# Kernel optimization log

Measured on AMD Instinct MI355X. Metric: run time of the kernel, lower is better.

Reference implementation:

```python
import jax, jax.numpy as jnp
import numpy as np

N, IN_DIM, OUT_DIM, HEADS, SUB = 4096, 256, 128, 4, 32
ETA = 0.5
LAMBDA_SPARSE = 0.05
NEG_BIG = -1e9


def setup_inputs() -> dict:
    key = jax.random.key(0)
    k1, k2, k3, k4 = jax.random.split(key, 4)
    H = jax.random.normal(k1, (N, IN_DIM), dtype=jnp.float32)
    # sparse binary adjacency mask (avg degree ~ 41) with self-loops
    adj_mask = (jax.random.uniform(k2, (N, N)) < 0.01).astype(jnp.float32)
    adj_mask = adj_mask.at[jnp.arange(N), jnp.arange(N)].set(1.0)
    # per-head orthonormal subspace bases U_k = QR(randn)[:, :SUB]
    raw = jax.random.normal(k3, (HEADS, IN_DIM, SUB), dtype=jnp.float32)
    U = jax.vmap(lambda r: jnp.linalg.qr(r)[0])(raw)  # [h, D, s]
    threshold = jnp.full((OUT_DIM,), LAMBDA_SPARSE, dtype=jnp.float32)
    proj_w = jax.random.normal(k4, (OUT_DIM, IN_DIM), dtype=jnp.float32) / np.float32(np.sqrt(IN_DIM))
    return {"H": H, "adj_mask": adj_mask, "U": U, "threshold": threshold, "proj_w": proj_w}


def reference(H, adj_mask, U, threshold, proj_w):
    # Z_k = U_k^T @ H^T  -> [h, s, N]
    Z = jnp.einsum('hds,nd->hsn', U, H)
    # scores_k = Z_k^T @ Z_k / sqrt(s)  -> [h, N, N]
    scores = jnp.einsum('hsn,hsm->hnm', Z, Z) / jnp.sqrt(jnp.float32(SUB))
    scores = scores + (1.0 - adj_mask)[None, :, :] * NEG_BIG
    alpha = jax.nn.softmax(scores, axis=-1)  # torch softmax(dim=1) on [N,N] rows
    # agg_k = Z_k @ alpha_k^T  -> [h, s, N];  sum_k U_k @ agg_k -> [D, N]
    agg = jnp.einsum('hsj,hij->hsi', Z, alpha)
    agg_sum = jnp.einsum('hds,hsn->dn', U, agg)
    H_half = H + ETA * agg_sum.T           # [N, D]
    H_half = H_half @ proj_w.T             # [N, out_dim]
    # soft-threshold
    H_out = jnp.sign(H_half) * jax.nn.relu(jnp.abs(H_half) - threshold[None, :])
    # orthogonality loss: sum_k ||U_k^T U_k - I||_F^2 + sum_{k<l} ||U_k^T U_l||_F^2
    G = jnp.einsum('kds,ldt->klst', U, U)  # [h, h, s, s]
    eye_s = jnp.eye(SUB, dtype=U.dtype)
    eye_h = jnp.eye(HEADS, dtype=U.dtype)
    sub = G - eye_h[:, :, None, None] * eye_s[None, None, :, :]
    sq = jnp.sum(sub ** 2, axis=(2, 3))    # [h, h]
    orth_loss = jnp.sum(jnp.triu(jnp.ones((HEADS, HEADS), dtype=U.dtype)) * sq)
    return H_out, orth_loss
```

## Files before the change

kernel.cpp:

```cpp
#include <hip/hip_runtime.h>
#include <hip/hip_bf16.h>
#include <math.h>

#define NN 4096
#define IN_DIM 256
#define OUT_DIM 128
#define HEADS 4
#define SUB 32
#define MAXDEG 128
#define ETA 0.5f
#define INV_SQRT_SUB 0.17677669529663687f

typedef __attribute__((ext_vector_type(8))) short bf16x8;
typedef __attribute__((ext_vector_type(4))) short s16x4;
typedef __attribute__((ext_vector_type(4))) float f32x4;

static __device__ inline short f2bf(float f) {
    unsigned u = __float_as_uint(f);
    unsigned r = u + 0x7FFFu + ((u >> 16) & 1u);
    return (short)(r >> 16);
}
static __device__ inline float bf2f(short s) {
    return __uint_as_float(((unsigned)(unsigned short)s) << 16);
}
#define MFMA16(a, b, c) __builtin_amdgcn_mfma_f32_16x16x32_bf16(a, b, c, 0, 0, 0)

__global__ __launch_bounds__(256) void fused_small(const float* __restrict__ U,
                                                   const float* __restrict__ PW,
                                                   const float* __restrict__ adj,
                                                   short* __restrict__ Wh,
                                                   short* __restrict__ Wl,
                                                   float* __restrict__ W2,
                                                   float* __restrict__ loss_parts,
                                                   int* __restrict__ nbr,
                                                   int* __restrict__ deg) {
    int b = blockIdx.x;
    int t = threadIdx.x;
    __shared__ float sh[260];
    __shared__ int cnt2[2];

    if (b < 256) {
        float v;
        if (b < 128) {
            int h = b >> 5, s = b & 31;
            v = U[h * IN_DIM * SUB + t * SUB + s];
        } else {
            v = PW[(b - 128) * IN_DIM + t];
        }
        short hi = f2bf(v);
        Wh[b * IN_DIM + t] = hi;
        Wl[b * IN_DIM + t] = f2bf(v - bf2f(hi));
    } else if (b < 384) {
        int hs = b - 256;
        int h = hs >> 5, s = hs & 31;
        sh[t] = U[h * IN_DIM * SUB + t * SUB + s];
        __syncthreads();
        if (t < 128) {
            const float4* pw4 = (const float4*)(PW + t * IN_DIM);
            const float4* u4  = (const float4*)sh;
            float acc = 0.f;
            #pragma unroll 4
            for (int d4 = 0; d4 < 64; ++d4) {
                float4 a = u4[d4], p = pw4[d4];
                acc += a.x * p.x + a.y * p.y + a.z * p.z + a.w * p.w;
            }
            W2[hs * OUT_DIM + t] = acc;
        }
    } else if (b < 394) {
        const int pk[10] = {0,0,0,0,1,1,1,2,2,3};
        const int pl[10] = {0,1,2,3,1,2,3,2,3,3};
        int p = b - 384;
        int k = pk[p], l = pl[p];
        int t2 = t & 31;
        int sg = t >> 5;
        const float* Uk = U + k * IN_DIM * SUB;
        const float* Ul = U + l * IN_DIM * SUB;
        float a0 = 0.f, a1 = 0.f, a2 = 0.f, a3 = 0.f;
        #pragma unroll 4
        for (int d = 0; d < IN_DIM; ++d) {
            float ul = Ul[d * SUB + t2];
            float u0 = Uk[d * SUB + sg * 4 + 0];
            float u1 = Uk[d * SUB + sg * 4 + 1];
            float u2 = Uk[d * SUB + sg * 4 + 2];
            float u3 = Uk[d * SUB + sg * 4 + 3];
            a0 += u0 * ul; a1 += u1 * ul; a2 += u2 * ul; a3 += u3 * ul;
        }
        if (k == l) {
            if (sg * 4 + 0 == t2) a0 -= 1.f;
            if (sg * 4 + 1 == t2) a1 -= 1.f;
            if (sg * 4 + 2 == t2) a2 -= 1.f;
            if (sg * 4 + 3 == t2) a3 -= 1.f;
        }
        float local = a0 * a0 + a1 * a1 + a2 * a2 + a3 * a3;
        local += __shfl_xor(local, 32, 64);
        local += __shfl_xor(local, 16, 64);
        local += __shfl_xor(local, 8, 64);
        local += __shfl_xor(local, 4, 64);
        local += __shfl_xor(local, 2, 64);
        local += __shfl_xor(local, 1, 64);
        if ((t & 63) == 0) sh[256 + (t >> 6)] = local;
        __syncthreads();
        if (t == 0) loss_parts[p] = sh[256] + sh[257] + sh[258] + sh[259];
    } else {
        int sb = b - 394;
        int half = t >> 7, u = t & 127;
        int row = sb * 2 + half;
        const float4* row4 = (const float4*)(adj + (size_t)row * NN);
        float4 v[8];
        #pragma unroll
        for (int k = 0; k < 8; ++k) v[k] = row4[u + k * 128];
        if (u == 0) cnt2[half] = 0;
        __syncthreads();
        int* nrow = nbr + row * MAXDEG;
        #pragma unroll
        for (int k = 0; k < 8; ++k) {
            int j0 = (u + k * 128) * 4;
            if (v[k].x > 0.5f) { int p = atomicAdd(&cnt2[half], 1); if (p < MAXDEG) nrow[p] = j0; }
            if (v[k].y > 0.5f) { int p = atomicAdd(&cnt2[half], 1); if (p < MAXDEG) nrow[p] = j0 + 1; }
            if (v[k].z > 0.5f) { int p = atomicAdd(&cnt2[half], 1); if (p < MAXDEG) nrow[p] = j0 + 2; }
            if (v[k].w > 0.5f) { int p = atomicAdd(&cnt2[half], 1); if (p < MAXDEG) nrow[p] = j0 + 3; }
        }
        __syncthreads();
        int dgr = cnt2[half] < MAXDEG ? cnt2[half] : MAXDEG;
        if (u >= dgr) nrow[u] = 0;
        if (u == 0) deg[row] = dgr;
    }
}

#define LDA 264
__global__ __launch_bounds__(256) void ztp_mfma(const float* __restrict__ H,
                                                const short* __restrict__ Wh,
                                                const short* __restrict__ Wl,
                                                float* __restrict__ ZT,
                                                float* __restrict__ P) {
    __shared__ short Ah[16 * LDA];
    __shared__ short Al[16 * LDA];
    int t = threadIdx.x, b = blockIdx.x;
    int m0 = (b >> 1) * 16, chalf = b & 1;

    {
        int r = t >> 4, dbase = (t & 15) * 16;
        const float4* src = (const float4*)(H + (size_t)(m0 + r) * IN_DIM + dbase);
        #pragma unroll
        for (int q = 0; q < 4; ++q) {
            float4 f = src[q];
            float fv[4] = {f.x, f.y, f.z, f.w};
            s16x4 hi, lo;
            #pragma unroll
            for (int j = 0; j < 4; ++j) {
                short h = f2bf(fv[j]);
                hi[j] = h;
                lo[j] = f2bf(fv[j] - bf2f(h));
            }
            *(s16x4*)&Ah[r * LDA + dbase + q * 4] = hi;
            *(s16x4*)&Al[r * LDA + dbase + q * 4] = lo;
        }
    }
    __syncthreads();

    int wave = t >> 6, lane = t & 63;
    int c0 = chalf * 128 + wave * 32;
    int arow = lane & 15, agrp = lane >> 4;

    const short* ahp = &Ah[arow * LDA + agrp * 8];
    const short* alp = &Al[arow * LDA + agrp * 8];
    const short* bh0 = Wh + (size_t)(c0 + arow) * IN_DIM + agrp * 8;
    const short* bl0 = Wl + (size_t)(c0 + arow) * IN_DIM + agrp * 8;
    const short* bh1 = bh0 + 16 * IN_DIM;
    const short* bl1 = bl0 + 16 * IN_DIM;

    f32x4 acc0 = {0.f, 0.f, 0.f, 0.f};
    f32x4 acc1 = {0.f, 0.f, 0.f, 0.f};

    #pragma unroll
    for (int kk = 0; kk < 8; ++kk) {
        int d0 = kk * 32;
        bf16x8 a_h = *(const bf16x8*)(ahp + d0);
        bf16x8 a_l = *(const bf16x8*)(alp + d0);
        bf16x8 b0h = *(const bf16x8*)(bh0 + d0);
        bf16x8 b0l = *(const bf16x8*)(bl0 + d0);
        bf16x8 b1h = *(const bf16x8*)(bh1 + d0);
        bf16x8 b1l = *(const bf16x8*)(bl1 + d0);
        acc0 = MFMA16(a_h, b0h, acc0);
        acc0 = MFMA16(a_h, b0l, acc0);
        acc0 = MFMA16(a_l, b0h, acc0);
        acc1 = MFMA16(a_h, b1h, acc1);
        acc1 = MFMA16(a_h, b1l, acc1);
        acc1 = MFMA16(a_l, b1h, acc1);
    }

    float* dst = chalf ? P : ZT;
    int colbase = c0 - chalf * 128;
    #pragma unroll
    for (int i = 0; i < 4; ++i) {
        int row = m0 + agrp * 4 + i;
        dst[(size_t)row * 128 + colbase + arow]      = acc0[i];
        dst[(size_t)row * 128 + colbase + 16 + arow] = acc1[i];
    }
}

__global__ __launch_bounds__(128) void attn_core(const float* __restrict__ ZT,
                                                 const float* __restrict__ Pm,
                                                 const float* __restrict__ W2,
                                                 const int* __restrict__ nbr,
                                                 const int* __restrict__ deg,
                                                 const float* __restrict__ threshold,
                                                 const float* __restrict__ loss_parts,
                                                 float* __restrict__ out) {
    int i = blockIdx.x;
    int t = threadIdx.x;
    __shared__ int   nbr_s[MAXDEG];
    __shared__ float e_s[MAXDEG][HEADS];
    __shared__ float z_s[128];
    __shared__ float agg_s[128];

    if (i == 0 && t == 0) {
        float L = 0.f;
        #pragma unroll
        for (int p = 0; p < 10; ++p) L += loss_parts[p];
        out[(size_t)NN * OUT_DIM] = L;
    }

    int dg = deg[i];
    int nb = nbr[i * MAXDEG + t];
    float zq = ZT[(size_t)i * 128 + t];
    float pval = Pm[(size_t)i * 128 + t];
    float th = threshold[t];

    nbr_s[t] = nb;
    z_s[t] = zq;
    __syncthreads();

    int jj0 = t >> 2, h = t & 3;
    int ntiles = (dg + 31) >> 5;
    const float4* qr = (const float4*)(&z_s[h * 32]);
    for (int tile = 0; tile < ntiles; ++tile) {
        int jj = tile * 32 + jj0;
        int j = nbr_s[jj];
        const float4* zr = (const float4*)(ZT + (size_t)j * 128 + h * 32);
        float acc = 0.f;
        #pragma unroll
        for (int k = 0; k < 8; ++k) {
            float4 z = zr[k];
            float4 q = qr[k];
            acc += z.x * q.x + z.y * q.y + z.z * q.z + z.w * q.w;
        }
        e_s[jj][h] = (jj < dg) ? __expf(acc * INV_SQRT_SUB) : 0.f;
    }
    __syncthreads();

    int hh = t >> 5;
    float accV = 0.f, accS = 0.f;
    const float* zbase = ZT + t;
    for (int jj = 0; jj < dg; jj += 8) {
        int j0 = nbr_s[jj],     j1 = nbr_s[jj + 1];
        int j2 = nbr_s[jj + 2], j3 = nbr_s[jj + 3];
        int j4 = nbr_s[jj + 4], j5 = nbr_s[jj + 5];
        int j6 = nbr_s[jj + 6], j7 = nbr_s[jj + 7];
        float v0 = zbase[(size_t)j0 * 128], v1 = zbase[(size_t)j1 * 128];
        float v2 = zbase[(size_t)j2 * 128], v3 = zbase[(size_t)j3 * 128];
        float v4 = zbase[(size_t)j4 * 128], v5 = zbase[(size_t)j5 * 128];
        float v6 = zbase[(size_t)j6 * 128], v7 = zbase[(size_t)j7 * 128];
        float e0 = e_s[jj][hh],     e1 = e_s[jj + 1][hh];
        float e2 = e_s[jj + 2][hh], e3 = e_s[jj + 3][hh];
        float e4 = e_s[jj + 4][hh], e5 = e_s[jj + 5][hh];
        float e6 = e_s[jj + 6][hh], e7 = e_s[jj + 7][hh];
        accV += e0 * v0 + e1 * v1 + e2 * v2 + e3 * v3
              + e4 * v4 + e5 * v5 + e6 * v6 + e7 * v7;
        accS += (e0 + e1) + (e2 + e3) + (e4 + e5) + (e6 + e7);
    }
    agg_s[t] = accV * (ETA / accS);
    __syncthreads();

    float val = pval;
    #pragma unroll 4
    for (int q4 = 0; q4 < 32; ++q4) {
        int hs = q4 * 4;
        float w0 = W2[(hs + 0) * 128 + t];
        float w1 = W2[(hs + 1) * 128 + t];
        float w2v = W2[(hs + 2) * 128 + t];
        float w3 = W2[(hs + 3) * 128 + t];
        float4 a = *(const float4*)&agg_s[hs];
        val += a.x * w0 + a.y * w1 + a.z * w2v + a.w * w3;
    }
    float av = fabsf(val) - th;
    out[(size_t)i * 128 + t] = (av > 0.f) ? copysignf(av, val) : 0.f;
}

extern "C" void kernel_launch(void* const* d_in, const int* in_sizes, int n_in,
                              void* d_out, int out_size, void* d_ws, size_t ws_size,
                              hipStream_t stream) {
    const float* H   = (const float*)d_in[0];
    const float* adj = (const float*)d_in[1];
    const float* U   = (const float*)d_in[2];
    const float* thr = (const float*)d_in[3];
    const float* PW  = (const float*)d_in[4];
    float* out = (float*)d_out;

    char* ws = (char*)d_ws;
    float* ZT    = (float*)(ws);
    float* P     = (float*)(ws + (size_t)2097152);
    float* W2    = (float*)(ws + (size_t)4194304);
    short* Wh    = (short*)(ws + (size_t)4259840);
    short* Wl    = (short*)(ws + (size_t)4390912);
    float* lossp = (float*)(ws + (size_t)4521984);
    int*   nbr   = (int*)  (ws + (size_t)4530176);
    int*   deg   = (int*)  (ws + (size_t)6627328);

    fused_small<<<394 + NN / 2, 256, 0, stream>>>(U, PW, adj, Wh, Wl, W2, lossp, nbr, deg);
    ztp_mfma<<<NN / 16 * 2, 256, 0, stream>>>(H, Wh, Wl, ZT, P);
    attn_core<<<NN, 128, 0, stream>>>(ZT, P, W2, nbr, deg, thr, lossp, out);
}
```

Baseline: 154.3 us.

## Fuse projection GEMM into front kernel with per-block weight split in LDS

Merges the weight bf16 hi/lo splitting and the H×[U|PW^T] MFMA projection into the front kernel, removing one kernel launch and the global Wh/Wl round-trip. Each block now converts its 32-column weight slice into LDS itself and converts H rows to hi/lo in registers straight from global memory, using 64-row tiles. The cost is redundant weight conversion in every block and larger LDS use per block, which can lower occupancy of the adjacency-scan blocks that share the kernel.

```diff
diff --git a/kernel.cpp b/kernel.cpp
--- a/kernel.cpp
+++ b/kernel.cpp
@@ -12,7 +12,6 @@
 #define INV_SQRT_SUB 0.17677669529663687f
 
 typedef __attribute__((ext_vector_type(8))) short bf16x8;
-typedef __attribute__((ext_vector_type(4))) short s16x4;
 typedef __attribute__((ext_vector_type(4))) float f32x4;
 
 static __device__ inline short f2bf(float f) {
@@ -25,33 +24,99 @@
 }
 #define MFMA16(a, b, c) __builtin_amdgcn_mfma_f32_16x16x32_bf16(a, b, c, 0, 0, 0)
 
-__global__ __launch_bounds__(256) void fused_small(const float* __restrict__ U,
-                                                   const float* __restrict__ PW,
-                                                   const float* __restrict__ adj,
-                                                   short* __restrict__ Wh,
-                                                   short* __restrict__ Wl,
-                                                   float* __restrict__ W2,
-                                                   float* __restrict__ loss_parts,
-                                                   int* __restrict__ nbr,
-                                                   int* __restrict__ deg) {
-    int b = blockIdx.x;
-    int t = threadIdx.x;
+#define BLD 264
+__global__ __launch_bounds__(256) void front(const float* __restrict__ H,
+                                             const float* __restrict__ U,
+                                             const float* __restrict__ PW,
+                                             const float* __restrict__ adj,
+                                             float* __restrict__ ZT,
+                                             float* __restrict__ P,
+                                             float* __restrict__ W2,
+                                             float* __restrict__ loss_parts,
+                                             int* __restrict__ nbr,
+                                             int* __restrict__ deg) {
+    int b = blockIdx.x, t = threadIdx.x;
+    __shared__ short Bh[32 * BLD];
+    __shared__ short Bl[32 * BLD];
     __shared__ float sh[260];
     __shared__ int cnt2[2];
 
-    if (b < 256) {
-        float v;
-        if (b < 128) {
-            int h = b >> 5, s = b & 31;
-            v = U[h * IN_DIM * SUB + t * SUB + s];
+    if (b < 512) {
+        int mtile = b >> 3, cblk = b & 7;
+        int m0 = mtile * 64;
+
+        if (cblk < 4) {
+            int s = t & 31, dgrp = t >> 5;
+            const float* ub = U + cblk * IN_DIM * SUB;
+            #pragma unroll 4
+            for (int k = 0; k < 32; ++k) {
+                int d = dgrp * 32 + k;
+                float v = ub[d * SUB + s];
+                short hi = f2bf(v);
+                Bh[s * BLD + d] = hi;
+                Bl[s * BLD + d] = f2bf(v - bf2f(hi));
+            }
         } else {
-            v = PW[(b - 128) * IN_DIM + t];
-        }
-        short hi = f2bf(v);
-        Wh[b * IN_DIM + t] = hi;
-        Wl[b * IN_DIM + t] = f2bf(v - bf2f(hi));
-    } else if (b < 384) {
-        int hs = b - 256;
+            int oo = t >> 3, o0 = (cblk - 4) * 32;
+            const float* pr = PW + (size_t)(o0 + oo) * IN_DIM + (t & 7) * 32;
+            #pragma unroll 4
+            for (int k = 0; k < 32; ++k) {
+                int d = (t & 7) * 32 + k;
+                float v = pr[k];
+                short hi = f2bf(v);
+                Bh[oo * BLD + d] = hi;
+                Bl[oo * BLD + d] = f2bf(v - bf2f(hi));
+            }
+        }
+        __syncthreads();
+
+        int w = t >> 6, lane = t & 63;
+        int arow = lane & 15, agrp = lane >> 4;
+        const float* hrow = H + (size_t)(m0 + w * 16 + arow) * IN_DIM;
+        const short* bh0 = &Bh[arow * BLD];
+        const short* bl0 = &Bl[arow * BLD];
+        const short* bh1 = &Bh[(16 + arow) * BLD];
+        const short* bl1 = &Bl[(16 + arow) * BLD];
+
+        f32x4 acc0 = {0.f, 0.f, 0.f, 0.f};
+        f32x4 acc1 = {0.f, 0.f, 0.f, 0.f};
+
+        #pragma unroll
+        for (int kk = 0; kk < 8; ++kk) {
+            int d0 = agrp * 8 + kk * 32;
+            float4 f0 = *(const float4*)(hrow + d0);
+            float4 f1 = *(const float4*)(hrow + d0 + 4);
+            float fv[8] = {f0.x, f0.y, f0.z, f0.w, f1.x, f1.y, f1.z, f1.w};
+            bf16x8 a_h, a_l;
+            #pragma unroll
+            for (int j = 0; j < 8; ++j) {
+                short hi = f2bf(fv[j]);
+                a_h[j] = hi;
+                a_l[j] = f2bf(fv[j] - bf2f(hi));
+            }
+            bf16x8 b0h = *(const bf16x8*)(bh0 + d0);
+            bf16x8 b0l = *(const bf16x8*)(bl0 + d0);
+            bf16x8 b1h = *(const bf16x8*)(bh1 + d0);
+            bf16x8 b1l = *(const bf16x8*)(bl1 + d0);
+            acc0 = MFMA16(a_h, b0h, acc0);
+            acc0 = MFMA16(a_h, b0l, acc0);
+            acc0 = MFMA16(a_l, b0h, acc0);
+            acc1 = MFMA16(a_h, b1h, acc1);
+            acc1 = MFMA16(a_h, b1l, acc1);
+            acc1 = MFMA16(a_l, b1h, acc1);
+        }
+
+        int c0 = cblk * 32;
+        float* dst = (c0 < 128) ? ZT : P;
+        int colbase = (c0 < 128) ? c0 : c0 - 128;
+        #pragma unroll
+        for (int i = 0; i < 4; ++i) {
+            int row = m0 + w * 16 + agrp * 4 + i;
+            dst[(size_t)row * 128 + colbase + arow]      = acc0[i];
+            dst[(size_t)row * 128 + colbase + 16 + arow] = acc1[i];
+        }
+    } else if (b < 640) {
+        int hs = b - 512;
         int h = hs >> 5, s = hs & 31;
         sh[t] = U[h * IN_DIM * SUB + t * SUB + s];
         __syncthreads();
@@ -66,10 +131,10 @@
             }
             W2[hs * OUT_DIM + t] = acc;
         }
-    } else if (b < 394) {
+    } else if (b < 650) {
         const int pk[10] = {0,0,0,0,1,1,1,2,2,3};
         const int pl[10] = {0,1,2,3,1,2,3,2,3,3};
-        int p = b - 384;
+        int p = b - 640;
         int k = pk[p], l = pl[p];
         int t2 = t & 31;
         int sg = t >> 5;
@@ -102,7 +167,7 @@
         __syncthreads();
         if (t == 0) loss_parts[p] = sh[256] + sh[257] + sh[258] + sh[259];
     } else {
-        int sb = b - 394;
+        int sb = b - 650;
         int half = t >> 7, u = t & 127;
         int row = sb * 2 + half;
         const float4* row4 = (const float4*)(adj + (size_t)row * NN);
@@ -124,78 +189,6 @@
         int dgr = cnt2[half] < MAXDEG ? cnt2[half] : MAXDEG;
         if (u >= dgr) nrow[u] = 0;
         if (u == 0) deg[row] = dgr;
-    }
-}
-
-#define LDA 264
-__global__ __launch_bounds__(256) void ztp_mfma(const float* __restrict__ H,
-                                                const short* __restrict__ Wh,
-                                                const short* __restrict__ Wl,
-                                                float* __restrict__ ZT,
-                                                float* __restrict__ P) {
-    __shared__ short Ah[16 * LDA];
-    __shared__ short Al[16 * LDA];
-    int t = threadIdx.x, b = blockIdx.x;
-    int m0 = (b >> 1) * 16, chalf = b & 1;
-
-    {
-        int r = t >> 4, dbase = (t & 15) * 16;
-        const float4* src = (const float4*)(H + (size_t)(m0 + r) * IN_DIM + dbase);
-        #pragma unroll
-        for (int q = 0; q < 4; ++q) {
-            float4 f = src[q];
-            float fv[4] = {f.x, f.y, f.z, f.w};
-            s16x4 hi, lo;
-            #pragma unroll
-            for (int j = 0; j < 4; ++j) {
-                short h = f2bf(fv[j]);
-                hi[j] = h;
-                lo[j] = f2bf(fv[j] - bf2f(h));
-            }
-            *(s16x4*)&Ah[r * LDA + dbase + q * 4] = hi;
-            *(s16x4*)&Al[r * LDA + dbase + q * 4] = lo;
-        }
-    }
-    __syncthreads();
-
-    int wave = t >> 6, lane = t & 63;
-    int c0 = chalf * 128 + wave * 32;
-    int arow = lane & 15, agrp = lane >> 4;
-
-    const short* ahp = &Ah[arow * LDA + agrp * 8];
-    const short* alp = &Al[arow * LDA + agrp * 8];
-    const short* bh0 = Wh + (size_t)(c0 + arow) * IN_DIM + agrp * 8;
-    const short* bl0 = Wl + (size_t)(c0 + arow) * IN_DIM + agrp * 8;
-    const short* bh1 = bh0 + 16 * IN_DIM;
-    const short* bl1 = bl0 + 16 * IN_DIM;
-
-    f32x4 acc0 = {0.f, 0.f, 0.f, 0.f};
-    f32x4 acc1 = {0.f, 0.f, 0.f, 0.f};
-
-    #pragma unroll
-    for (int kk = 0; kk < 8; ++kk) {
-        int d0 = kk * 32;
-        bf16x8 a_h = *(const bf16x8*)(ahp + d0);
-        bf16x8 a_l = *(const bf16x8*)(alp + d0);
-        bf16x8 b0h = *(const bf16x8*)(bh0 + d0);
-        bf16x8 b0l = *(const bf16x8*)(bl0 + d0);
-        bf16x8 b1h = *(const bf16x8*)(bh1 + d0);
-        bf16x8 b1l = *(const bf16x8*)(bl1 + d0);
-        acc0 = MFMA16(a_h, b0h, acc0);
-        acc0 = MFMA16(a_h, b0l, acc0);
-        acc0 = MFMA16(a_l, b0h, acc0);
-        acc1 = MFMA16(a_h, b1h, acc1);
-        acc1 = MFMA16(a_h, b1l, acc1);
-        acc1 = MFMA16(a_l, b1h, acc1);
-    }
-
-    float* dst = chalf ? P : ZT;
-    int colbase = c0 - chalf * 128;
-    #pragma unroll
-    for (int i = 0; i < 4; ++i) {
-        int row = m0 + agrp * 4 + i;
-        dst[(size_t)row * 128 + colbase + arow]      = acc0[i];
-        dst[(size_t)row * 128 + colbase + 16 + arow] = acc1[i];
     }
 }
 
@@ -301,13 +294,10 @@
     float* ZT    = (float*)(ws);
     float* P     = (float*)(ws + (size_t)2097152);
     float* W2    = (float*)(ws + (size_t)4194304);
-    short* Wh    = (short*)(ws + (size_t)4259840);
-    short* Wl    = (short*)(ws + (size_t)4390912);
     float* lossp = (float*)(ws + (size_t)4521984);
     int*   nbr   = (int*)  (ws + (size_t)4530176);
     int*   deg   = (int*)  (ws + (size_t)6627328);
 
-    fused_small<<<394 + NN / 2, 256, 0, stream>>>(U, PW, adj, Wh, Wl, W2, lossp, nbr, deg);
-    ztp_mfma<<<NN / 16 * 2, 256, 0, stream>>>(H, Wh, Wl, ZT, P);
+    front<<<650 + NN / 2, 256, 0, stream>>>(H, U, PW, adj, ZT, P, W2, lossp, nbr, deg);
     attn_core<<<NN, 128, 0, stream>>>(ZT, P, W2, nbr, deg, thr, lossp, out);
 }
```

Result: faster. 148.2 us (-4.0%).
